# Optimization experiments

Measured on AMD Instinct MI355X. Metric: run time of the kernel, lower is better.

Reference implementation:

```python
import jax, jax.numpy as jnp
import numpy as np

V, D, H, L, E, DH, K, PMAX = 50257, 128, 4, 4, 8, 512, 2, 256
B, T = 8, 256


def setup_inputs() -> dict:
    key = jax.random.key(0)
    ks = jax.random.split(key, 10)
    s = 0.02
    def n(k, shape):
        return jax.random.normal(k, shape, jnp.float32) * s
    return dict(
        idx=jax.random.randint(ks[0], (B, T), 0, V),
        tok_emb=n(ks[1], (V, D)),
        pos_emb=n(ks[2], (PMAX, D)),
        ln1_g=jnp.ones((L, D), jnp.float32), ln1_b=jnp.zeros((L, D), jnp.float32),
        in_w=n(ks[3], (L, 3 * D, D)), in_b=jnp.zeros((L, 3 * D), jnp.float32),
        out_w=n(ks[4], (L, D, D)), out_b=jnp.zeros((L, D), jnp.float32),
        ln2_g=jnp.ones((L, D), jnp.float32), ln2_b=jnp.zeros((L, D), jnp.float32),
        gate_w=n(ks[5], (L, E, D)),
        w1=n(ks[6], (L, E, DH, D)),
        w2=n(ks[7], (L, E, D, DH)),
        lnf_g=jnp.ones((D,), jnp.float32), lnf_b=jnp.zeros((D,), jnp.float32),
        lm_w=n(ks[8], (V, D)),
    )


def _ln(x, g, b):
    mu = x.mean(-1, keepdims=True)
    var = jnp.var(x, -1, keepdims=True)
    return (x - mu) / jnp.sqrt(var + 1e-5) * g + b


def _moe(x, gw, w1, w2):
    # x: [N, D]; top-2 sparse MoE, computed densely per expert then combined.
    logits = x @ gw.T                              # [N, E]
    probs = jax.nn.softmax(logits, -1)
    topw, topi = jax.lax.top_k(probs, K)           # [N, K]
    topw = topw / topw.sum(-1, keepdims=True)
    we = (topw[..., None] * jax.nn.one_hot(topi, E, dtype=x.dtype)).sum(1)  # [N, E]
    h = jax.nn.silu(jnp.einsum('nd,ehd->neh', x, w1))   # [N, E, DH]
    y = jnp.einsum('neh,edh->ned', h, w2)               # [N, E, D]
    return jnp.einsum('ned,ne->nd', y, we)


def reference(idx, tok_emb, pos_emb, ln1_g, ln1_b, in_w, in_b, out_w, out_b,
              ln2_g, ln2_b, gate_w, w1, w2, lnf_g, lnf_b, lm_w):
    b, t = idx.shape
    x = tok_emb[idx] + pos_emb[:t]                 # [B, T, D]
    dh = D // H
    scale = 1.0 / np.sqrt(dh)
    for l in range(L):
        xl = _ln(x, ln1_g[l], ln1_b[l])
        qkv = xl @ in_w[l].T + in_b[l]
        q, k, v = jnp.split(qkv, 3, -1)
        q = q.reshape(b, t, H, dh)
        k = k.reshape(b, t, H, dh)
        v = v.reshape(b, t, H, dh)
        att = jax.nn.softmax(jnp.einsum('bqhd,bkhd->bhqk', q, k) * scale, -1)
        o = jnp.einsum('bhqk,bkhd->bqhd', att, v).reshape(b, t, D)
        x = x + o @ out_w[l].T + out_b[l]
        x2 = _ln(x, ln2_g[l], ln2_b[l]).reshape(b * t, D)
        x = x + _moe(x2, gate_w[l], w1[l], w2[l]).reshape(b, t, D)
    return _ln(x, lnf_g, lnf_b) @ lm_w.T           # [B, T, V]
```

## Files before the change

### kernel.cpp

```cpp
#include <hip/hip_runtime.h>
#include <math.h>

#define NTOK 2048
#define DD   128
#define NHEAD 4
#define DHEAD 32
#define NLAYER 4
#define NEXP 8
#define DHID 512
#define NVOCAB 50257
#define VPAD  50304
#define SEQ   256
#define NBATCH 8

typedef __attribute__((ext_vector_type(8))) short short8v;
typedef __attribute__((ext_vector_type(4))) float f32x4;

__device__ __forceinline__ unsigned short nm_bf16r(float f) {
  unsigned u = __float_as_uint(f);
  u += 0x7fffu + ((u >> 16) & 1u);
  return (unsigned short)(u >> 16);
}

__device__ __forceinline__ float nm_silu(float a) {
  return a / (1.f + __expf(-a));
}

template<int N4>
__device__ __forceinline__ float nm_dotv(const float* __restrict__ a,
                                         const float* __restrict__ w) {
  const float4* a4 = (const float4*)a;
  const float4* w4 = (const float4*)w;
  float sx = 0.f, sy = 0.f, sz = 0.f, sw = 0.f;
#pragma unroll 16
  for (int k = 0; k < N4; ++k) {
    float4 av = a4[k], wv = w4[k];
    sx = fmaf(av.x, wv.x, sx);
    sy = fmaf(av.y, wv.y, sy);
    sz = fmaf(av.z, wv.z, sz);
    sw = fmaf(av.w, wv.w, sw);
  }
  return (sx + sy) + (sz + sw);
}

#define C3_LMW 6438912ull
#define C3_W1  6963200ull
#define C3_ALL 7487488ull
#define CVTB   7312
__global__ __launch_bounds__(256) void nm_init(
    const int* __restrict__ idx, const float* __restrict__ tok,
    const float* __restrict__ pos, const float* __restrict__ g,
    const float* __restrict__ b, const float* __restrict__ lmw,
    const float* __restrict__ w1l3, const float* __restrict__ w2l3,
    float* __restrict__ x, float* __restrict__ xl,
    unsigned short* __restrict__ lmwb, unsigned short* __restrict__ w1b3,
    unsigned short* __restrict__ w2b3, int* __restrict__ zp) {
  int bid = blockIdx.x, tid = threadIdx.x;
  if (bid < CVTB) {
    size_t base = ((size_t)bid * 256 + tid) * 4;
    if (base < (size_t)NVOCAB * DD) {
      float4 v = *(const float4*)(lmw + base);
      ushort4 us = {nm_bf16r(v.x), nm_bf16r(v.y), nm_bf16r(v.z), nm_bf16r(v.w)};
      *(ushort4*)(lmwb + base) = us;
    } else if (base < C3_LMW) {
      ushort4 us = {0, 0, 0, 0};
      *(ushort4*)(lmwb + base) = us;
    } else if (base < C3_W1) {
      size_t j = base - C3_LMW;
      float4 v = *(const float4*)(w1l3 + j);
      ushort4 us = {nm_bf16r(v.x), nm_bf16r(v.y), nm_bf16r(v.z), nm_bf16r(v.w)};
      *(ushort4*)(w1b3 + j) = us;
    } else {
      size_t j = base - C3_W1;
      float4 v = *(const float4*)(w2l3 + j);
      ushort4 us = {nm_bf16r(v.x), nm_bf16r(v.y), nm_bf16r(v.z), nm_bf16r(v.w)};
      *(ushort4*)(w2b3 + j) = us;
    }
  } else if (bid < CVTB + NTOK / 4) {
    int n = (bid - CVTB) * 4 + (tid >> 6);
    int lane = tid & 63;
    int t = idx[n];
    float v0 = tok[(size_t)t * DD + lane]      + pos[(n % SEQ) * DD + lane];
    float v1 = tok[(size_t)t * DD + lane + 64] + pos[(n % SEQ) * DD + lane + 64];
    x[n * DD + lane]      = v0;
    x[n * DD + lane + 64] = v1;
    float s = v0 + v1;
#pragma unroll
    for (int o = 32; o > 0; o >>= 1) s += __shfl_xor(s, o, 64);
    float mu = s * (1.f / 128.f);
    float d0 = v0 - mu, d1 = v1 - mu;
    float q = d0 * d0 + d1 * d1;
#pragma unroll
    for (int o = 32; o > 0; o >>= 1) q += __shfl_xor(q, o, 64);
    float rstd = rsqrtf(q * (1.f / 128.f) + 1e-5f);
    xl[n * DD + lane]      = d0 * rstd * g[lane]      + b[lane];
    xl[n * DD + lane + 64] = d1 * rstd * g[lane + 64] + b[lane + 64];
  } else {
    if (tid < 68) zp[tid] = 0;
  }
}

__global__ void nm_embed_ln(const int* __restrict__ idx, const float* __restrict__ tok,
                            const float* __restrict__ pos, const float* __restrict__ g,
                            const float* __restrict__ b, float* __restrict__ x,
                            float* __restrict__ xlf) {
  int n = blockIdx.x, lane = threadIdx.x;
  int t = idx[n];
  float v0 = tok[(size_t)t * DD + lane]      + pos[(n % SEQ) * DD + lane];
  float v1 = tok[(size_t)t * DD + lane + 64] + pos[(n % SEQ) * DD + lane + 64];
  x[n * DD + lane]      = v0;
  x[n * DD + lane + 64] = v1;
  float s = v0 + v1;
#pragma unroll
  for (int o = 32; o > 0; o >>= 1) s += __shfl_xor(s, o, 64);
  float mu = s * (1.f / 128.f);
  float d0 = v0 - mu, d1 = v1 - mu;
  float q = d0 * d0 + d1 * d1;
#pragma unroll
  for (int o = 32; o > 0; o >>= 1) q += __shfl_xor(q, o, 64);
  float rstd = rsqrtf(q * (1.f / 128.f) + 1e-5f);
  xlf[n * DD + lane]      = d0 * rstd * g[lane]      + b[lane];
  xlf[n * DD + lane + 64] = d1 * rstd * g[lane + 64] + b[lane + 64];
}

__global__ void nm_ln(const float* __restrict__ in, const float* __restrict__ g,
                      const float* __restrict__ b, float* __restrict__ out) {
  int n = blockIdx.x, lane = threadIdx.x;
  float v0 = in[n * DD + lane], v1 = in[n * DD + lane + 64];
  float s = v0 + v1;
#pragma unroll
  for (int o = 32; o > 0; o >>= 1) s += __shfl_xor(s, o, 64);
  float mu = s * (1.f / 128.f);
  float d0 = v0 - mu, d1 = v1 - mu;
  float q = d0 * d0 + d1 * d1;
#pragma unroll
  for (int o = 32; o > 0; o >>= 1) q += __shfl_xor(q, o, 64);
  float rstd = rsqrtf(q * (1.f / 128.f) + 1e-5f);
  out[n * DD + lane]      = d0 * rstd * g[lane]      + b[lane];
  out[n * DD + lane + 64] = d1 * rstd * g[lane + 64] + b[lane + 64];
}

__global__ void nm_combine_ln(const float* __restrict__ yb, const int* __restrict__ posm,
                              const float* __restrict__ topw, float* __restrict__ x,
                              const float* __restrict__ g, const float* __restrict__ b,
                              float* __restrict__ xl, unsigned short* __restrict__ xb) {
  int n = blockIdx.x, lane = threadIdx.x;
  float w0 = topw[2 * n], w1 = topw[2 * n + 1];
  int p0 = posm[2 * n], p1 = posm[2 * n + 1];
  float v0 = x[n * DD + lane]      + w0 * yb[(size_t)p0 * DD + lane]
                                   + w1 * yb[(size_t)p1 * DD + lane];
  float v1 = x[n * DD + lane + 64] + w0 * yb[(size_t)p0 * DD + lane + 64]
                                   + w1 * yb[(size_t)p1 * DD + lane + 64];
  x[n * DD + lane]      = v0;
  x[n * DD + lane + 64] = v1;
  float s = v0 + v1;
#pragma unroll
  for (int o = 32; o > 0; o >>= 1) s += __shfl_xor(s, o, 64);
  float mu = s * (1.f / 128.f);
  float d0 = v0 - mu, d1 = v1 - mu;
  float q = d0 * d0 + d1 * d1;
#pragma unroll
  for (int o = 32; o > 0; o >>= 1) q += __shfl_xor(q, o, 64);
  float rstd = rsqrtf(q * (1.f / 128.f) + 1e-5f);
  float o0 = d0 * rstd * g[lane]      + b[lane];
  float o1 = d1 * rstd * g[lane + 64] + b[lane + 64];
  xl[n * DD + lane]      = o0;
  xl[n * DD + lane + 64] = o1;
  if (xb) {
    xb[n * DD + lane]      = nm_bf16r(o0);
    xb[n * DD + lane + 64] = nm_bf16r(o1);
  }
}

template<int F, int MT>
__global__ __launch_bounds__(256) void nm_gemm2(
    const float* __restrict__ A, const float* __restrict__ B,
    float* __restrict__ C, const float* __restrict__ bias,
    int M, int N, int K,
    const int* __restrict__ list, const int* __restrict__ cnt,
    const int* __restrict__ off) {
  constexpr bool GA = F & 1, SI = F & 2, BI = F & 4, GR = F & 16;
  constexpr int RG = MT / 64;
  __shared__ __align__(16) float As[64][MT + 4];
  __shared__ __align__(16) float Bs[64][68];
  int tid = threadIdx.x;
  int n0 = blockIdx.x * 64, m0 = blockIdx.y * MT;
  int Mloc = M, o = 0;
  const float* Bb = B;
  if constexpr (GR) {
    int e = blockIdx.z;
    Mloc = cnt[e];
    if (m0 >= Mloc) return;
    o = off[e];
    Bb = B + (size_t)e * (size_t)N * K;
  }
  int tm = tid & 15, tn = tid >> 4;
  float acc[RG * 4][4] = {};
  for (int kc = 0; kc < K; kc += 64) {
#pragma unroll
    for (int i = 0; i < RG * 4; ++i) {
      int f = tid + 256 * i;
      int r = f >> 4, c4 = f & 15;
      int mi = m0 + r;
      if (mi >= Mloc) mi = m0;
      const float* ar;
      if constexpr (GA) ar = A + (size_t)(list[o + mi] >> 1) * K;
      else              ar = A + (size_t)(o + mi) * K;
      float4 v = *(const float4*)(ar + kc + c4 * 4);
      int k = c4 * 4;
      As[k][r] = v.x; As[k + 1][r] = v.y; As[k + 2][r] = v.z; As[k + 3][r] = v.w;
    }
#pragma unroll
    for (int i = 0; i < 4; ++i) {
      int f = tid + 256 * i;
      int r = f >> 4, c4 = f & 15;
      const float* br = Bb + (size_t)(n0 + r) * K + kc + c4 * 4;
      float4 v = *(const float4*)br;
      int k = c4 * 4;
      Bs[k][r] = v.x; Bs[k + 1][r] = v.y; Bs[k + 2][r] = v.z; Bs[k + 3][r] = v.w;
    }
    __syncthreads();
#pragma unroll 16
    for (int k = 0; k < 64; ++k) {
      float4 b = *(const float4*)&Bs[k][tn * 4];
#pragma unroll
      for (int g2 = 0; g2 < RG; ++g2) {
        float4 a = *(const float4*)&As[k][g2 * 64 + tm * 4];
        acc[g2*4+0][0] = fmaf(a.x, b.x, acc[g2*4+0][0]);
        acc[g2*4+0][1] = fmaf(a.x, b.y, acc[g2*4+0][1]);
        acc[g2*4+0][2] = fmaf(a.x, b.z, acc[g2*4+0][2]);
        acc[g2*4+0][3] = fmaf(a.x, b.w, acc[g2*4+0][3]);
        acc[g2*4+1][0] = fmaf(a.y, b.x, acc[g2*4+1][0]);
        acc[g2*4+1][1] = fmaf(a.y, b.y, acc[g2*4+1][1]);
        acc[g2*4+1][2] = fmaf(a.y, b.z, acc[g2*4+1][2]);
        acc[g2*4+1][3] = fmaf(a.y, b.w, acc[g2*4+1][3]);
        acc[g2*4+2][0] = fmaf(a.z, b.x, acc[g2*4+2][0]);
        acc[g2*4+2][1] = fmaf(a.z, b.y, acc[g2*4+2][1]);
        acc[g2*4+2][2] = fmaf(a.z, b.z, acc[g2*4+2][2]);
        acc[g2*4+2][3] = fmaf(a.z, b.w, acc[g2*4+2][3]);
        acc[g2*4+3][0] = fmaf(a.w, b.x, acc[g2*4+3][0]);
        acc[g2*4+3][1] = fmaf(a.w, b.y, acc[g2*4+3][1]);
        acc[g2*4+3][2] = fmaf(a.w, b.z, acc[g2*4+3][2]);
        acc[g2*4+3][3] = fmaf(a.w, b.w, acc[g2*4+3][3]);
      }
    }
    __syncthreads();
  }
  float4 bv = {0.f, 0.f, 0.f, 0.f};
  if constexpr (BI) bv = *(const float4*)(bias + n0 + tn * 4);
#pragma unroll
  for (int g2 = 0; g2 < RG; ++g2) {
#pragma unroll
    for (int i = 0; i < 4; ++i) {
      int row = m0 + g2 * 64 + tm * 4 + i;
      if (GR && row >= Mloc) continue;
      float* cr = C + (size_t)(o + row) * N + n0 + tn * 4;
      float r0 = acc[g2 * 4 + i][0], r1 = acc[g2 * 4 + i][1];
      float r2 = acc[g2 * 4 + i][2], r3 = acc[g2 * 4 + i][3];
      if constexpr (BI) { r0 += bv.x; r1 += bv.y; r2 += bv.z; r3 += bv.w; }
      if constexpr (SI) { r0 = nm_silu(r0); r1 = nm_silu(r1); r2 = nm_silu(r2); r3 = nm_silu(r3); }
      float4 st = {r0, r1, r2, r3};
      *(float4*)cr = st;
    }
  }
}

template<int F, int KK>
__global__ __launch_bounds__(256) void nm_bgemm(
    const unsigned short* __restrict__ A, const unsigned short* __restrict__ B,
    float* __restrict__ Cf, unsigned short* __restrict__ Cb,
    const float* __restrict__ bias, int M, int N,
    const int* __restrict__ list, const int* __restrict__ cnt,
    const int* __restrict__ off) {
  constexpr bool GA = F & 1, SI = F & 2, BI = F & 4, SB = F & 8, GR = F & 16;
  int wave = threadIdx.x >> 6, lane = threadIdx.x & 63;
  int n0 = blockIdx.x * 32;
  int m0 = blockIdx.y * 128 + wave * 32;
  int Mloc = M, o = 0;
  const unsigned short* Bb = B;
  if constexpr (GR) {
    int e = blockIdx.z;
    Mloc = cnt[e];
    o = off[e];
    Bb = B + (size_t)e * (size_t)N * KK;
  }
  if (m0 >= Mloc) return;
  int lr = lane & 15, lk = (lane >> 4) * 8;
  const unsigned short* arow[2];
#pragma unroll
  for (int i = 0; i < 2; ++i) {
    int mi = m0 + i * 16 + lr;
    if (mi >= Mloc) mi = Mloc - 1;
    int r = GA ? (list[o + mi] >> 1) : (o + mi);
    arow[i] = A + (size_t)r * KK;
  }
  const unsigned short* brow[2] = { Bb + (size_t)(n0 + lr) * KK,
                                    Bb + (size_t)(n0 + 16 + lr) * KK };
  f32x4 acc[2][2] = {};
#pragma unroll
  for (int ks = 0; ks < KK / 32; ++ks) {
    int kb = ks * 32 + lk;
    short8v a0 = *(const short8v*)(arow[0] + kb);
    short8v a1 = *(const short8v*)(arow[1] + kb);
    short8v b0 = *(const short8v*)(brow[0] + kb);
    short8v b1 = *(const short8v*)(brow[1] + kb);
    acc[0][0] = __builtin_amdgcn_mfma_f32_16x16x32_bf16(a0, b0, acc[0][0], 0, 0, 0);
    acc[0][1] = __builtin_amdgcn_mfma_f32_16x16x32_bf16(a0, b1, acc[0][1], 0, 0, 0);
    acc[1][0] = __builtin_amdgcn_mfma_f32_16x16x32_bf16(a1, b0, acc[1][0], 0, 0, 0);
    acc[1][1] = __builtin_amdgcn_mfma_f32_16x16x32_bf16(a1, b1, acc[1][1], 0, 0, 0);
  }
  float bc[2] = {0.f, 0.f};
  if constexpr (BI) {
    bc[0] = bias[n0 + (lane & 15)];
    bc[1] = bias[n0 + 16 + (lane & 15)];
  }
#pragma unroll
  for (int i = 0; i < 2; ++i) {
    int rbase = m0 + i * 16 + (lane >> 4) * 4;
#pragma unroll
    for (int r = 0; r < 4; ++r) {
      int row = rbase + r;
      if (GR && row >= Mloc) continue;
#pragma unroll
      for (int j = 0; j < 2; ++j) {
        float v = acc[i][j][r];
        if constexpr (BI) v += bc[j];
        if constexpr (SI) v = nm_silu(v);
        int col = n0 + j * 16 + (lane & 15);
        if constexpr (SB) Cb[(size_t)(o + row) * N + col] = nm_bf16r(v);
        else              Cf[(size_t)(o + row) * N + col] = v;
      }
    }
  }
}

__global__ __launch_bounds__(256) void nm_oplng(
    const float* __restrict__ ao, const float* __restrict__ w,
    const float* __restrict__ bias, float* __restrict__ x,
    const float* __restrict__ g, const float* __restrict__ b,
    float* __restrict__ xlf, unsigned short* __restrict__ xlb,
    const float* __restrict__ gw,
    int* __restrict__ topi, float* __restrict__ topw, int* __restrict__ cnt,
    int* __restrict__ ticket, int* __restrict__ off, int* __restrict__ list,
    int* __restrict__ posm) {
  __shared__ __align__(16) float As[64][36];
  __shared__ __align__(16) float Bs[64][132];
  __shared__ float Ls[32][9];
  __shared__ int doR;
  __shared__ int cv[NEXP], lcur[NEXP];
  int tid = threadIdx.x;
  int m0 = blockIdx.x * 32;
  int tm = tid >> 5, tn = tid & 31;
  float acc[4][4] = {};
  for (int kc = 0; kc < DD; kc += 64) {
#pragma unroll
    for (int i = 0; i < 2; ++i) {
      int ch = tid + 256 * i, r = ch >> 4, c4 = ch & 15;
      float4 v = *(const float4*)(ao + (size_t)(m0 + r) * DD + kc + c4 * 4);
      int k = c4 * 4;
      As[k][r] = v.x; As[k + 1][r] = v.y; As[k + 2][r] = v.z; As[k + 3][r] = v.w;
    }
#pragma unroll
    for (int i = 0; i < 8; ++i) {
      int ch = tid + 256 * i, r = ch >> 4, c4 = ch & 15;
      float4 v = *(const float4*)(w + (size_t)r * DD + kc + c4 * 4);
      int k = c4 * 4;
      Bs[k][r] = v.x; Bs[k + 1][r] = v.y; Bs[k + 2][r] = v.z; Bs[k + 3][r] = v.w;
    }
    __syncthreads();
#pragma unroll 8
    for (int k = 0; k < 64; ++k) {
      float4 a = *(const float4*)&As[k][tm * 4];
      float4 bb = *(const float4*)&Bs[k][tn * 4];
      acc[0][0] = fmaf(a.x, bb.x, acc[0][0]); acc[0][1] = fmaf(a.x, bb.y, acc[0][1]);
      acc[0][2] = fmaf(a.x, bb.z, acc[0][2]); acc[0][3] = fmaf(a.x, bb.w, acc[0][3]);
      acc[1][0] = fmaf(a.y, bb.x, acc[1][0]); acc[1][1] = fmaf(a.y, bb.y, acc[1][1]);
      acc[1][2] = fmaf(a.y, bb.z, acc[1][2]); acc[1][3] = fmaf(a.y, bb.w, acc[1][3]);
      acc[2][0] = fmaf(a.z, bb.x, acc[2][0]); acc[2][1] = fmaf(a.z, bb.y, acc[2][1]);
      acc[2][2] = fmaf(a.z, bb.z, acc[2][2]); acc[2][3] = fmaf(a.z, bb.w, acc[2][3]);
      acc[3][0] = fmaf(a.w, bb.x, acc[3][0]); acc[3][1] = fmaf(a.w, bb.y, acc[3][1]);
      acc[3][2] = fmaf(a.w, bb.z, acc[3][2]); acc[3][3] = fmaf(a.w, bb.w, acc[3][3]);
    }
    __syncthreads();
  }
  float4 bv = *(const float4*)(bias + tn * 4);
  float rr[4][4], s1[4], s2[4];
#pragma unroll
  for (int i = 0; i < 4; ++i) {
    int rw = m0 + tm * 4 + i;
    float4 xv = *(const float4*)(x + (size_t)rw * DD + tn * 4);
    float r0 = acc[i][0] + bv.x + xv.x;
    float r1 = acc[i][1] + bv.y + xv.y;
    float r2 = acc[i][2] + bv.z + xv.z;
    float r3 = acc[i][3] + bv.w + xv.w;
    rr[i][0] = r0; rr[i][1] = r1; rr[i][2] = r2; rr[i][3] = r3;
    float4 st = {r0, r1, r2, r3};
    *(float4*)(x + (size_t)rw * DD + tn * 4) = st;
    s1[i] = r0 + r1 + r2 + r3;
    s2[i] = r0 * r0 + r1 * r1 + r2 * r2 + r3 * r3;
  }
#pragma unroll
  for (int o = 16; o >= 1; o >>= 1) {
#pragma unroll
    for (int i = 0; i < 4; ++i) {
      s1[i] += __shfl_xor(s1[i], o, 64);
      s2[i] += __shfl_xor(s2[i], o, 64);
    }
  }
  float4 gv  = *(const float4*)(g + tn * 4);
  float4 bbv = *(const float4*)(b + tn * 4);
#pragma unroll
  for (int i = 0; i < 4; ++i) {
    int rw = m0 + tm * 4 + i;
    float mu = s1[i] * (1.f / 128.f);
    float var = s2[i] * (1.f / 128.f) - mu * mu;
    float rstd = rsqrtf(var + 1e-5f);
    float y0 = (rr[i][0] - mu) * rstd * gv.x + bbv.x;
    float y1 = (rr[i][1] - mu) * rstd * gv.y + bbv.y;
    float y2 = (rr[i][2] - mu) * rstd * gv.z + bbv.z;
    float y3 = (rr[i][3] - mu) * rstd * gv.w + bbv.w;
    float4 yv = {y0, y1, y2, y3};
    if (xlf) *(float4*)(xlf + (size_t)rw * DD + tn * 4) = yv;
    if (xlb) {
      ushort4 us = {nm_bf16r(y0), nm_bf16r(y1), nm_bf16r(y2), nm_bf16r(y3)};
      *(ushort4*)(xlb + (size_t)rw * DD + tn * 4) = us;
    }
    *(float4*)&Bs[tm * 4 + i][tn * 4] = yv;
  }
  __syncthreads();
  int grow = tid >> 3, ge = tid & 7;
  const float4* xr = (const float4*)&Bs[grow][0];
  const float4* wr = (const float4*)(gw + (size_t)ge * DD);
  float sx = 0.f, sy = 0.f, sz = 0.f, sw = 0.f;
#pragma unroll
  for (int k2 = 0; k2 < 32; ++k2) {
    float4 a = xr[k2], w4 = wr[k2];
    sx = fmaf(a.x, w4.x, sx); sy = fmaf(a.y, w4.y, sy);
    sz = fmaf(a.z, w4.z, sz); sw = fmaf(a.w, w4.w, sw);
  }
  Ls[grow][ge] = (sx + sy) + (sz + sw);
  __syncthreads();
  if (ge == 0) {
    float gl[NEXP];
#pragma unroll
    for (int e = 0; e < NEXP; ++e) gl[e] = Ls[grow][e];
    int i0 = 0;
#pragma unroll
    for (int e = 1; e < NEXP; ++e) if (gl[e] > gl[i0]) i0 = e;
    int i1 = (i0 == 0) ? 1 : 0;
#pragma unroll
    for (int e = 0; e < NEXP; ++e) { if (e != i0 && gl[e] > gl[i1]) i1 = e; }
    float p1 = __expf(gl[i1] - gl[i0]);
    float inv = 1.f / (1.f + p1);
    int n = m0 + grow;
    topi[2 * n] = i0; topi[2 * n + 1] = i1;
    topw[2 * n] = inv; topw[2 * n + 1] = p1 * inv;
    atomicAdd(cnt + i0, 1);
    atomicAdd(cnt + i1, 1);
  }
  __syncthreads();
  if (tid == 0) {
    __threadfence();
    doR = (atomicAdd(ticket, 1) == 63);
    if (doR) __threadfence();
  }
  __syncthreads();
  if (doR) {
    if (tid < NEXP) cv[tid] = atomicAdd(cnt + tid, 0);
    __syncthreads();
    if (tid < NEXP) {
      int o2 = 0;
      for (int e = 0; e < tid; ++e) o2 += cv[e];
      lcur[tid] = o2;
      off[tid] = o2;
    }
    __syncthreads();
    for (int t = tid; t < 2 * NTOK; t += 256) {
      int e = topi[t];
      int p = atomicAdd(&lcur[e], 1);
// ... 42 lines not shown
    float sc = 0.f;
#pragma unroll
    for (int k = 0; k < 8; ++k) {
      float4 v = kr[k];
      sc += qv[4*k]*v.x + qv[4*k+1]*v.y + qv[4*k+2]*v.z + qv[4*k+3]*v.w;
    }
    sc *= scale;
    float mn = fmaxf(m, sc);
    float f = __expf(m - mn), p = __expf(sc - mn);
    s = s * f + p;
    const float4* vr = (const float4*)Vs[j];
#pragma unroll
    for (int k = 0; k < 8; ++k) {
      float4 v = vr[k];
      acc[4*k]   = acc[4*k]  * f + p * v.x;
      acc[4*k+1] = acc[4*k+1]* f + p * v.y;
      acc[4*k+2] = acc[4*k+2]* f + p * v.z;
      acc[4*k+3] = acc[4*k+3]* f + p * v.w;
    }
    m = mn;
  }
  mbuf[q][slot] = m;
  sbuf[q][slot] = s;
  __syncthreads();
  float M = mbuf[q][0];
#pragma unroll
  for (int t = 1; t < 8; ++t) M = fmaxf(M, mbuf[q][t]);
  float S = 0.f;
#pragma unroll
  for (int t = 0; t < 8; ++t) S += sbuf[q][t] * __expf(mbuf[q][t] - M);
  float w = __expf(m - M);
#pragma unroll
  for (int d = 0; d < DHEAD; ++d) acc[d] *= w;
#pragma unroll
  for (int p = 0; p < 8; ++p) {
    if (slot == p) {
      if (p == 0) {
#pragma unroll
        for (int d = 0; d < DHEAD; ++d) accbuf[q][d] = acc[d];
      } else {
#pragma unroll
        for (int d = 0; d < DHEAD; ++d) accbuf[q][d] += acc[d];
      }
    }
    __syncthreads();
  }
  if (slot == 0) sbuf[q][8] = 1.f / S;
  __syncthreads();
  int q2 = tid >> 3, c4 = tid & 7;
  float inv = sbuf[q2][8];
  float4 v = *(const float4*)&accbuf[q2][c4 * 4];
  v.x *= inv; v.y *= inv; v.z *= inv; v.w *= inv;
  *(float4*)(o + (size_t)(b * SEQ + qt * 32 + q2) * DD + h * DHEAD + c4 * 4) = v;
}

__global__ void nm_qkv(const float* __restrict__ xl, const float* __restrict__ w,
                       const float* __restrict__ bias, float* __restrict__ qkv) {
  __shared__ __align__(16) float xs[DD];
  int n = blockIdx.x, tid = threadIdx.x;
  xs[tid] = xl[n * DD + tid];
  __syncthreads();
#pragma unroll
  for (int jj = 0; jj < 3; ++jj) {
    int j = tid + jj * 128;
    qkv[(size_t)n * 384 + j] = nm_dotv<32>(xs, w + (size_t)j * DD) + bias[j];
  }
}

__global__ void nm_outproj(const float* __restrict__ ao, const float* __restrict__ w,
                           const float* __restrict__ bias, float* __restrict__ x) {
  __shared__ __align__(16) float os[DD];
  int n = blockIdx.x, tid = threadIdx.x;
  os[tid] = ao[n * DD + tid];
  __syncthreads();
  x[n * DD + tid] += nm_dotv<32>(os, w + (size_t)tid * DD) + bias[tid];
}

__global__ void nm_moe(const float* __restrict__ x2, const float* __restrict__ gw,
                       const float* __restrict__ w1, const float* __restrict__ w2,
                       float* __restrict__ x) {
  __shared__ __align__(16) float xs[DD];
  __shared__ __align__(16) float hs[DHID];
  __shared__ float gl[NEXP];
  __shared__ int   ei[2];
  __shared__ float ew[2];
  int n = blockIdx.x, tid = threadIdx.x;
  if (tid < DD) xs[tid] = x2[n * DD + tid];
  __syncthreads();
  if (tid < NEXP) gl[tid] = nm_dotv<32>(xs, gw + (size_t)tid * DD);
  __syncthreads();
  if (tid == 0) {
    int i0 = 0;
#pragma unroll
    for (int e = 1; e < NEXP; ++e) if (gl[e] > gl[i0]) i0 = e;
    int i1 = (i0 == 0) ? 1 : 0;
    for (int e = 0; e < NEXP; ++e) { if (e == i0) continue; if (gl[e] > gl[i1]) i1 = e; }
    float p1 = __expf(gl[i1] - gl[i0]);
    float inv = 1.f / (1.f + p1);
    ei[0] = i0; ei[1] = i1; ew[0] = inv; ew[1] = p1 * inv;
  }
  __syncthreads();
  float yacc = 0.f;
  for (int t2 = 0; t2 < 2; ++t2) {
    int e = ei[t2];
    float wt = ew[t2];
    const float* w1e = w1 + (size_t)e * DHID * DD;
// ... 114 lines not shown
#pragma unroll
  for (int j = 0; j < 4; ++j)
#pragma unroll
    for (int i = 0; i < 4; ++i)
#pragma unroll
      for (int r = 0; r < 4; ++r)
        Cs[(wr * 64 + i * 16 + hi4 + r) * 132 + wc * 64 + j * 16 + lr] = acc[i][j][r];
  __syncthreads();
  bool full = (col0 + 128 <= NVOCAB);
#pragma unroll 4
  for (int rr = 0; rr < 32; ++rr) {
    int row = wave * 32 + rr;
    float v0 = Cs[row * 132 + lane];
    float v1 = Cs[row * 132 + 64 + lane];
    size_t base = (size_t)(row0 + row) * NVOCAB + col0;
    if (full) {
      out[base + lane] = v0;
      out[base + 64 + lane] = v1;
    } else {
      if (col0 + lane < NVOCAB)      out[base + lane] = v0;
      if (col0 + 64 + lane < NVOCAB) out[base + 64 + lane] = v1;
    }
  }
}

extern "C" void kernel_launch(void* const* d_in, const int* in_sizes, int n_in,
                              void* d_out, int out_size, void* d_ws, size_t ws_size,
                              hipStream_t stream) {
  const int*   idx   = (const int*)  d_in[0];
  const float* tok   = (const float*)d_in[1];
  const float* pos   = (const float*)d_in[2];
  const float* ln1g  = (const float*)d_in[3];
  const float* ln1b  = (const float*)d_in[4];
  const float* inw   = (const float*)d_in[5];
  const float* inb   = (const float*)d_in[6];
  const float* outw  = (const float*)d_in[7];
  const float* outb  = (const float*)d_in[8];
  const float* ln2g  = (const float*)d_in[9];
  const float* ln2b  = (const float*)d_in[10];
  const float* gatew = (const float*)d_in[11];
  const float* w1    = (const float*)d_in[12];
  const float* w2    = (const float*)d_in[13];
  const float* lnfg  = (const float*)d_in[14];
  const float* lnfb  = (const float*)d_in[15];
  const float* lmw   = (const float*)d_in[16];
  float* out = (float*)d_out;

  float* ws   = (float*)d_ws;
  float* x    = ws;
  float* xl   = x    + NTOK * DD;
  float* qkv  = xl   + NTOK * DD;
  float* ao   = qkv  + NTOK * 384;
  float* topw = ao   + NTOK * DD;
  float* H    = topw + 2 * NTOK;
  float* yb   = H    + 2 * NTOK * DHID;
  int*   topi = (int*)(yb + 2 * NTOK * DD);
  int*   list = topi + 2 * NTOK;
  int*   posm = list + 2 * NTOK;
  int*   cnt  = posm + 2 * NTOK;
  int*   offs = cnt  + NLAYER * NEXP;
  int*   tick = offs + NLAYER * NEXP;
  unsigned short* xlb  = (unsigned short*)(tick + 8);
  unsigned short* Hb   = xlb + NTOK * DD;
  unsigned short* xfb  = Hb  + 2 * NTOK * DHID;
  unsigned short* w1b3 = xfb + NTOK * DD;
  unsigned short* w2b3 = w1b3 + NEXP * DHID * DD;
  unsigned short* lmwb = w2b3 + NEXP * DD * DHID;
  const size_t need = (size_t)((char*)(lmwb + (size_t)VPAD * DD) - (char*)d_ws);
  const bool pre = (ws_size >= need);

  const float* w1l3 = w1 + (size_t)3 * NEXP * DHID * DD;
  const float* w2l3 = w2 + (size_t)3 * NEXP * DD * DHID;

  if (pre) {
    nm_init<<<CVTB + NTOK / 4 + 1, 256, 0, stream>>>(
        idx, tok, pos, ln1g, ln1b, lmw, w1l3, w2l3, x, xl, lmwb, w1b3, w2b3, cnt);
    for (int l = 0; l < NLAYER; ++l) {
      nm_gemm2<4, 128><<<dim3(384 / 64, NTOK / 128), 256, 0, stream>>>(
          xl, inw + (size_t)l * 384 * DD, qkv, inb + (size_t)l * 384,
          NTOK, 384, DD, nullptr, nullptr, nullptr);
      nm_attn2<<<dim3(NBATCH * NHEAD, SEQ / 32), 256, 0, stream>>>(qkv, ao);
      nm_oplng<<<NTOK / 32, 256, 0, stream>>>(
          ao, outw + (size_t)l * DD * DD, outb + (size_t)l * DD, x,
          ln2g + l * DD, ln2b + l * DD, xl, (l == 3) ? xlb : (unsigned short*)nullptr,
          gatew + (size_t)l * NEXP * DD, topi, topw, cnt + l * NEXP,
          tick + l, offs + l * NEXP, list, posm);
      int* cnt_l = cnt + l * NEXP;
      int* off_l = offs + l * NEXP;
      if (l < 3) {
        const float* w1l = w1 + (size_t)l * NEXP * DHID * DD;
        const float* w2l = w2 + (size_t)l * NEXP * DD * DHID;
        nm_gemm2<19, 128><<<dim3(DHID / 64, 2 * NTOK / 128, NEXP), 256, 0, stream>>>(
            xl, w1l, H, nullptr, 0, DHID, DD, list, cnt_l, off_l);
        nm_gemm2<16, 64><<<dim3(DD / 64, 2 * NTOK / 64, NEXP), 256, 0, stream>>>(
            H, w2l, yb, nullptr, 0, DD, DHID, nullptr, cnt_l, off_l);
      } else {
        nm_bgemm<27, 128><<<dim3(DHID / 32, 32, NEXP), 256, 0, stream>>>(
            xlb, w1b3, nullptr, Hb, nullptr, 0, DHID, list, cnt_l, off_l);
        nm_bgemm<16, 512><<<dim3(DD / 32, 32, NEXP), 256, 0, stream>>>(
            Hb, w2b3, yb, nullptr, nullptr, 0, DD, nullptr, cnt_l, off_l);
      }
      const float* gN = (l < NLAYER - 1) ? ln1g + (l + 1) * DD : lnfg;
      const float* bN = (l < NLAYER - 1) ? ln1b + (l + 1) * DD : lnfb;
      nm_combine_ln<<<NTOK, 64, 0, stream>>>(
          yb, posm, topw, x, gN, bN, xl,
          (l == NLAYER - 1) ? xfb : (unsigned short*)nullptr);
    }
    nm_lmhead2<<<dim3(VPAD / 128, NTOK / 128), 256, 0, stream>>>(xfb, lmwb, out);
  } else {
    nm_embed_ln<<<NTOK, 64, 0, stream>>>(idx, tok, pos, ln1g, ln1b, x, xl);
    for (int l = 0; l < NLAYER; ++l) {
      nm_qkv<<<NTOK, 128, 0, stream>>>(xl, inw + (size_t)l * 384 * DD,
                                       inb + (size_t)l * 384, qkv);
      nm_attn2<<<dim3(NBATCH * NHEAD, SEQ / 32), 256, 0, stream>>>(qkv, ao);
      nm_outproj<<<NTOK, 128, 0, stream>>>(ao, outw + (size_t)l * DD * DD,
                                           outb + (size_t)l * DD, x);
      nm_ln<<<NTOK, 64, 0, stream>>>(x, ln2g + l * DD, ln2b + l * DD, xl);
      nm_moe<<<NTOK, 256, 0, stream>>>(xl, gatew + (size_t)l * NEXP * DD,
                                       w1 + (size_t)l * NEXP * DHID * DD,
                                       w2 + (size_t)l * NEXP * DD * DHID, x);
      const float* gN = (l < NLAYER - 1) ? ln1g + (l + 1) * DD : lnfg;
      const float* bN = (l < NLAYER - 1) ? ln1b + (l + 1) * DD : lnfb;
      nm_ln<<<NTOK, 64, 0, stream>>>(x, gN, bN, xl);
    }
    nm_lmhead_f32<<<dim3(VPAD / 128, NTOK / 128), 256, 0, stream>>>(xl, lmw, out);
  }
}
```

Before: 828.4 us.

## Fuse combine+LN with QKV projection and expert FFN into single MoE kernel

```diff
diff --git a/kernel.cpp b/kernel.cpp
--- a/kernel.cpp
+++ b/kernel.cpp
@@ -43,18 +43,14 @@
   return (sx + sy) + (sz + sw);
 }
 
-#define C3_LMW 6438912ull
-#define C3_W1  6963200ull
-#define C3_ALL 7487488ull
-#define CVTB   7312
+#define CVT_N 6438912ull
+#define CVTB  6288
 __global__ __launch_bounds__(256) void nm_init(
     const int* __restrict__ idx, const float* __restrict__ tok,
     const float* __restrict__ pos, const float* __restrict__ g,
     const float* __restrict__ b, const float* __restrict__ lmw,
-    const float* __restrict__ w1l3, const float* __restrict__ w2l3,
     float* __restrict__ x, float* __restrict__ xl,
-    unsigned short* __restrict__ lmwb, unsigned short* __restrict__ w1b3,
-    unsigned short* __restrict__ w2b3, int* __restrict__ zp) {
+    unsigned short* __restrict__ lmwb, int* __restrict__ zp) {
   int bid = blockIdx.x, tid = threadIdx.x;
   if (bid < CVTB) {
     size_t base = ((size_t)bid * 256 + tid) * 4;
@@ -62,19 +58,9 @@
       float4 v = *(const float4*)(lmw + base);
       ushort4 us = {nm_bf16r(v.x), nm_bf16r(v.y), nm_bf16r(v.z), nm_bf16r(v.w)};
       *(ushort4*)(lmwb + base) = us;
-    } else if (base < C3_LMW) {
+    } else {
       ushort4 us = {0, 0, 0, 0};
       *(ushort4*)(lmwb + base) = us;
-    } else if (base < C3_W1) {
-      size_t j = base - C3_LMW;
-      float4 v = *(const float4*)(w1l3 + j);
-      ushort4 us = {nm_bf16r(v.x), nm_bf16r(v.y), nm_bf16r(v.z), nm_bf16r(v.w)};
-      *(ushort4*)(w1b3 + j) = us;
-    } else {
-      size_t j = base - C3_W1;
-      float4 v = *(const float4*)(w2l3 + j);
-      ushort4 us = {nm_bf16r(v.x), nm_bf16r(v.y), nm_bf16r(v.z), nm_bf16r(v.w)};
-      *(ushort4*)(w2b3 + j) = us;
     }
   } else if (bid < CVTB + NTOK / 4) {
     int n = (bid - CVTB) * 4 + (tid >> 6);
@@ -96,241 +82,147 @@
     xl[n * DD + lane]      = d0 * rstd * g[lane]      + b[lane];
     xl[n * DD + lane + 64] = d1 * rstd * g[lane + 64] + b[lane + 64];
   } else {
-    if (tid < 68) zp[tid] = 0;
-  }
-}
-
-__global__ void nm_embed_ln(const int* __restrict__ idx, const float* __restrict__ tok,
-                            const float* __restrict__ pos, const float* __restrict__ g,
-                            const float* __restrict__ b, float* __restrict__ x,
-                            float* __restrict__ xlf) {
-  int n = blockIdx.x, lane = threadIdx.x;
-  int t = idx[n];
-  float v0 = tok[(size_t)t * DD + lane]      + pos[(n % SEQ) * DD + lane];
-  float v1 = tok[(size_t)t * DD + lane + 64] + pos[(n % SEQ) * DD + lane + 64];
-  x[n * DD + lane]      = v0;
-  x[n * DD + lane + 64] = v1;
-  float s = v0 + v1;
-#pragma unroll
-  for (int o = 32; o > 0; o >>= 1) s += __shfl_xor(s, o, 64);
-  float mu = s * (1.f / 128.f);
-  float d0 = v0 - mu, d1 = v1 - mu;
-  float q = d0 * d0 + d1 * d1;
-#pragma unroll
-  for (int o = 32; o > 0; o >>= 1) q += __shfl_xor(q, o, 64);
-  float rstd = rsqrtf(q * (1.f / 128.f) + 1e-5f);
-  xlf[n * DD + lane]      = d0 * rstd * g[lane]      + b[lane];
-  xlf[n * DD + lane + 64] = d1 * rstd * g[lane + 64] + b[lane + 64];
-}
-
-__global__ void nm_ln(const float* __restrict__ in, const float* __restrict__ g,
-                      const float* __restrict__ b, float* __restrict__ out) {
-  int n = blockIdx.x, lane = threadIdx.x;
-  float v0 = in[n * DD + lane], v1 = in[n * DD + lane + 64];
-  float s = v0 + v1;
-#pragma unroll
-  for (int o = 32; o > 0; o >>= 1) s += __shfl_xor(s, o, 64);
-  float mu = s * (1.f / 128.f);
-  float d0 = v0 - mu, d1 = v1 - mu;
-  float q = d0 * d0 + d1 * d1;
-#pragma unroll
-  for (int o = 32; o > 0; o >>= 1) q += __shfl_xor(q, o, 64);
-  float rstd = rsqrtf(q * (1.f / 128.f) + 1e-5f);
-  out[n * DD + lane]      = d0 * rstd * g[lane]      + b[lane];
-  out[n * DD + lane + 64] = d1 * rstd * g[lane + 64] + b[lane + 64];
-}
-
-__global__ void nm_combine_ln(const float* __restrict__ yb, const int* __restrict__ posm,
-                              const float* __restrict__ topw, float* __restrict__ x,
-                              const float* __restrict__ g, const float* __restrict__ b,
-                              float* __restrict__ xl, unsigned short* __restrict__ xb) {
-  int n = blockIdx.x, lane = threadIdx.x;
-  float w0 = topw[2 * n], w1 = topw[2 * n + 1];
-  int p0 = posm[2 * n], p1 = posm[2 * n + 1];
-  float v0 = x[n * DD + lane]      + w0 * yb[(size_t)p0 * DD + lane]
-                                   + w1 * yb[(size_t)p1 * DD + lane];
-  float v1 = x[n * DD + lane + 64] + w0 * yb[(size_t)p0 * DD + lane + 64]
-                                   + w1 * yb[(size_t)p1 * DD + lane + 64];
-  x[n * DD + lane]      = v0;
-  x[n * DD + lane + 64] = v1;
-  float s = v0 + v1;
-#pragma unroll
-  for (int o = 32; o > 0; o >>= 1) s += __shfl_xor(s, o, 64);
-  float mu = s * (1.f / 128.f);
-  float d0 = v0 - mu, d1 = v1 - mu;
-  float q = d0 * d0 + d1 * d1;
-#pragma unroll
-  for (int o = 32; o > 0; o >>= 1) q += __shfl_xor(q, o, 64);
-  float rstd = rsqrtf(q * (1.f / 128.f) + 1e-5f);
-  float o0 = d0 * rstd * g[lane]      + b[lane];
-  float o1 = d1 * rstd * g[lane + 64] + b[lane + 64];
-  xl[n * DD + lane]      = o0;
-  xl[n * DD + lane + 64] = o1;
-  if (xb) {
-    xb[n * DD + lane]      = nm_bf16r(o0);
-    xb[n * DD + lane + 64] = nm_bf16r(o1);
-  }
-}
-
-template<int F, int MT>
-__global__ __launch_bounds__(256) void nm_gemm2(
-    const float* __restrict__ A, const float* __restrict__ B,
-    float* __restrict__ C, const float* __restrict__ bias,
-    int M, int N, int K,
-    const int* __restrict__ list, const int* __restrict__ cnt,
-    const int* __restrict__ off) {
-  constexpr bool GA = F & 1, SI = F & 2, BI = F & 4, GR = F & 16;
-  constexpr int RG = MT / 64;
-  __shared__ __align__(16) float As[64][MT + 4];
-  __shared__ __align__(16) float Bs[64][68];
+    if (tid < 72) zp[tid] = 0;
+  }
+}
+
+template<int MODE>
+__global__ __launch_bounds__(256) void nm_cqkv(
+    const float* __restrict__ yb, const int* __restrict__ posm,
+    const float* __restrict__ topw, float* __restrict__ x,
+    const float* __restrict__ xlin, const float* __restrict__ g,
+    const float* __restrict__ b, unsigned short* __restrict__ xfb,
+    const float* __restrict__ w, const float* __restrict__ bias,
+    float* __restrict__ qkv) {
+  __shared__ __align__(16) float xs[32][132];
+  __shared__ __align__(16) float qs[(MODE < 2) ? 32 * 388 : 4];
   int tid = threadIdx.x;
-  int n0 = blockIdx.x * 64, m0 = blockIdx.y * MT;
-  int Mloc = M, o = 0;
-  const float* Bb = B;
-  if constexpr (GR) {
-    int e = blockIdx.z;
-    Mloc = cnt[e];
-    if (m0 >= Mloc) return;
-    o = off[e];
-    Bb = B + (size_t)e * (size_t)N * K;
-  }
-  int tm = tid & 15, tn = tid >> 4;
-  float acc[RG * 4][4] = {};
-  for (int kc = 0; kc < K; kc += 64) {
-#pragma unroll
-    for (int i = 0; i < RG * 4; ++i) {
-      int f = tid + 256 * i;
-      int r = f >> 4, c4 = f & 15;
-      int mi = m0 + r;
-      if (mi >= Mloc) mi = m0;
-      const float* ar;
-      if constexpr (GA) ar = A + (size_t)(list[o + mi] >> 1) * K;
-      else              ar = A + (size_t)(o + mi) * K;
-      float4 v = *(const float4*)(ar + kc + c4 * 4);
-      int k = c4 * 4;
-      As[k][r] = v.x; As[k + 1][r] = v.y; As[k + 2][r] = v.z; As[k + 3][r] = v.w;
-    }
+  int n0 = blockIdx.x * 32;
+  int r = tid >> 3, p = tid & 7;
+  int n = n0 + r;
+  float4 a0, a1, a2, a3;
+  if constexpr (MODE == 0) {
+    const float* xr = xlin + (size_t)n * DD + p * 16;
+    a0 = *(const float4*)(xr + 0);  a1 = *(const float4*)(xr + 4);
+    a2 = *(const float4*)(xr + 8);  a3 = *(const float4*)(xr + 12);
 #pragma unroll
     for (int i = 0; i < 4; ++i) {
-      int f = tid + 256 * i;
-      int r = f >> 4, c4 = f & 15;
-      const float* br = Bb + (size_t)(n0 + r) * K + kc + c4 * 4;
-      float4 v = *(const float4*)br;
-      int k = c4 * 4;
-      Bs[k][r] = v.x; Bs[k + 1][r] = v.y; Bs[k + 2][r] = v.z; Bs[k + 3][r] = v.w;
-    }
-    __syncthreads();
-#pragma unroll 16
-    for (int k = 0; k < 64; ++k) {
-      float4 b = *(const float4*)&Bs[k][tn * 4];
-#pragma unroll
-      for (int g2 = 0; g2 < RG; ++g2) {
-        float4 a = *(const float4*)&As[k][g2 * 64 + tm * 4];
-        acc[g2*4+0][0] = fmaf(a.x, b.x, acc[g2*4+0][0]);
-        acc[g2*4+0][1] = fmaf(a.x, b.y, acc[g2*4+0][1]);
-        acc[g2*4+0][2] = fmaf(a.x, b.z, acc[g2*4+0][2]);
-        acc[g2*4+0][3] = fmaf(a.x, b.w, acc[g2*4+0][3]);
-        acc[g2*4+1][0] = fmaf(a.y, b.x, acc[g2*4+1][0]);
-        acc[g2*4+1][1] = fmaf(a.y, b.y, acc[g2*4+1][1]);
-        acc[g2*4+1][2] = fmaf(a.y, b.z, acc[g2*4+1][2]);
-        acc[g2*4+1][3] = fmaf(a.y, b.w, acc[g2*4+1][3]);
-        acc[g2*4+2][0] = fmaf(a.z, b.x, acc[g2*4+2][0]);
-        acc[g2*4+2][1] = fmaf(a.z, b.y, acc[g2*4+2][1]);
-        acc[g2*4+2][2] = fmaf(a.z, b.z, acc[g2*4+2][2]);
-        acc[g2*4+2][3] = fmaf(a.z, b.w, acc[g2*4+2][3]);
-        acc[g2*4+3][0] = fmaf(a.w, b.x, acc[g2*4+3][0]);
-        acc[g2*4+3][1] = fmaf(a.w, b.y, acc[g2*4+3][1]);
-        acc[g2*4+3][2] = fmaf(a.w, b.z, acc[g2*4+3][2]);
-        acc[g2*4+3][3] = fmaf(a.w, b.w, acc[g2*4+3][3]);
+      ((float4*)&xs[r][p * 16])[i] = (i == 0) ? a0 : (i == 1) ? a1 : (i == 2) ? a2 : a3;
+    }
+  } else {
+    float* xr = x + (size_t)n * DD + p * 16;
+    a0 = *(const float4*)(xr + 0);  a1 = *(const float4*)(xr + 4);
+    a2 = *(const float4*)(xr + 8);  a3 = *(const float4*)(xr + 12);
+    float w0 = topw[2 * n], w1 = topw[2 * n + 1];
+    int p0 = posm[2 * n], p1 = posm[2 * n + 1];
+    const float* y0 = yb + (size_t)p0 * DD + p * 16;
+    const float* y1 = yb + (size_t)p1 * DD + p * 16;
+#pragma unroll
+    for (int i = 0; i < 4; ++i) {
+      float4 u0 = ((const float4*)y0)[i];
+      float4 u1 = ((const float4*)y1)[i];
+      float4* ai = (i == 0) ? &a0 : (i == 1) ? &a1 : (i == 2) ? &a2 : &a3;
+      ai->x += w0 * u0.x + w1 * u1.x;
+      ai->y += w0 * u0.y + w1 * u1.y;
+      ai->z += w0 * u0.z + w1 * u1.z;
+      ai->w += w0 * u0.w + w1 * u1.w;
+    }
+    if constexpr (MODE == 1) {
+      ((float4*)xr)[0] = a0; ((float4*)xr)[1] = a1;
+      ((float4*)xr)[2] = a2; ((float4*)xr)[3] = a3;
+    }
+    float s1 = (a0.x + a0.y + a0.z + a0.w) + (a1.x + a1.y + a1.z + a1.w)
+             + (a2.x + a2.y + a2.z + a2.w) + (a3.x + a3.y + a3.z + a3.w);
+    float s2 = a0.x*a0.x + a0.y*a0.y + a0.z*a0.z + a0.w*a0.w
+             + a1.x*a1.x + a1.y*a1.y + a1.z*a1.z + a1.w*a1.w
+             + a2.x*a2.x + a2.y*a2.y + a2.z*a2.z + a2.w*a2.w
+             + a3.x*a3.x + a3.y*a3.y + a3.z*a3.z + a3.w*a3.w;
+#pragma unroll
+    for (int o = 4; o >= 1; o >>= 1) {
+      s1 += __shfl_xor(s1, o, 8);
+      s2 += __shfl_xor(s2, o, 8);
+    }
+    float mu = s1 * (1.f / 128.f);
+    float var = s2 * (1.f / 128.f) - mu * mu;
+    float rstd = rsqrtf(var + 1e-5f);
+    const float4* gp = (const float4*)(g + p * 16);
+    const float4* bp = (const float4*)(b + p * 16);
+#pragma unroll
+    for (int i = 0; i < 4; ++i) {
+      float4 gv = gp[i], bv = bp[i];
+      float4* ai = (i == 0) ? &a0 : (i == 1) ? &a1 : (i == 2) ? &a2 : &a3;
+      float4 yv = {(ai->x - mu) * rstd * gv.x + bv.x,
+                   (ai->y - mu) * rstd * gv.y + bv.y,
+                   (ai->z - mu) * rstd * gv.z + bv.z,
+                   (ai->w - mu) * rstd * gv.w + bv.w};
+      if constexpr (MODE == 2) {
+        ushort4 us = {nm_bf16r(yv.x), nm_bf16r(yv.y), nm_bf16r(yv.z), nm_bf16r(yv.w)};
+        *(ushort4*)(xfb + (size_t)n * DD + p * 16 + i * 4) = us;
+      } else {
+        ((float4*)&xs[r][p * 16])[i] = yv;
       }
     }
-    __syncthreads();
-  }
-  float4 bv = {0.f, 0.f, 0.f, 0.f};
-  if constexpr (BI) bv = *(const float4*)(bias + n0 + tn * 4);
-#pragma unroll
-  for (int g2 = 0; g2 < RG; ++g2) {
-#pragma unroll
-    for (int i = 0; i < 4; ++i) {
-      int row = m0 + g2 * 64 + tm * 4 + i;
-      if (GR && row >= Mloc) continue;
-      float* cr = C + (size_t)(o + row) * N + n0 + tn * 4;
-      float r0 = acc[g2 * 4 + i][0], r1 = acc[g2 * 4 + i][1];
-      float r2 = acc[g2 * 4 + i][2], r3 = acc[g2 * 4 + i][3];
-      if constexpr (BI) { r0 += bv.x; r1 += bv.y; r2 += bv.z; r3 += bv.w; }
-      if constexpr (SI) { r0 = nm_silu(r0); r1 = nm_silu(r1); r2 = nm_silu(r2); r3 = nm_silu(r3); }
-      float4 st = {r0, r1, r2, r3};
-      *(float4*)cr = st;
-    }
-  }
-}
-
-template<int F, int KK>
-__global__ __launch_bounds__(256) void nm_bgemm(
-    const unsigned short* __restrict__ A, const unsigned short* __restrict__ B,
-    float* __restrict__ Cf, unsigned short* __restrict__ Cb,
-    const float* __restrict__ bias, int M, int N,
-    const int* __restrict__ list, const int* __restrict__ cnt,
-    const int* __restrict__ off) {
-  constexpr bool GA = F & 1, SI = F & 2, BI = F & 4, SB = F & 8, GR = F & 16;
-  int wave = threadIdx.x >> 6, lane = threadIdx.x & 63;
-  int n0 = blockIdx.x * 32;
-  int m0 = blockIdx.y * 128 + wave * 32;
-  int Mloc = M, o = 0;
-  const unsigned short* Bb = B;
-  if constexpr (GR) {
-    int e = blockIdx.z;
-    Mloc = cnt[e];
-    o = off[e];
-    Bb = B + (size_t)e * (size_t)N * KK;
-  }
-  if (m0 >= Mloc) return;
-  int lr = lane & 15, lk = (lane >> 4) * 8;
-  const unsigned short* arow[2];
+  }
+  if constexpr (MODE == 2) return;
+  __syncthreads();
+  float* qsf = (float*)qs;
+#pragma unroll 8
+  for (int i = 0; i < 48; ++i) {
+    int pp = i * 256 + tid;
+    int col = pp >> 5, tk = pp & 31;
+    float v = nm_dotv<32>(&xs[tk][0], w + (size_t)col * DD) + bias[col];
+    qsf[tk * 388 + col] = v;
+  }
+  __syncthreads();
+#pragma unroll
+  for (int i = 0; i < 12; ++i) {
+    int e4 = i * 256 + tid;
+    int tk = e4 / 96, c4 = e4 % 96;
+    float4 v = *(const float4*)&qsf[tk * 388 + c4 * 4];
+    *(float4*)(qkv + (size_t)(n0 + tk) * 384 + c4 * 4) = v;
+  }
+}
+
+__global__ __launch_bounds__(256) void nm_moe_f(
+    const float* __restrict__ xl, const float* __restrict__ w1,
+    const float* __restrict__ w2, const int* __restrict__ list,
+    const int* __restrict__ cnt, const int* __restrict__ off,
+    float* __restrict__ yb) {
+  __shared__ __align__(16) float xs[16][132];
+  __shared__ __align__(16) float Hs[16][516];
+  int e = blockIdx.y;
+  int c = cnt[e];
+  int m0 = blockIdx.x * 16;
+  if (m0 >= c) return;
+  int o = off[e];
+  const float* w1e = w1 + (size_t)e * DHID * DD;
+  const float* w2e = w2 + (size_t)e * DD * DHID;
+  int tid = threadIdx.x;
 #pragma unroll
   for (int i = 0; i < 2; ++i) {
-    int mi = m0 + i * 16 + lr;
-    if (mi >= Mloc) mi = Mloc - 1;
-    int r = GA ? (list[o + mi] >> 1) : (o + mi);
-    arow[i] = A + (size_t)r * KK;
-  }
-  const unsigned short* brow[2] = { Bb + (size_t)(n0 + lr) * KK,
-                                    Bb + (size_t)(n0 + 16 + lr) * KK };
-  f32x4 acc[2][2] = {};
-#pragma unroll
-  for (int ks = 0; ks < KK / 32; ++ks) {
-    int kb = ks * 32 + lk;
-    short8v a0 = *(const short8v*)(arow[0] + kb);
-    short8v a1 = *(const short8v*)(arow[1] + kb);
-    short8v b0 = *(const short8v*)(brow[0] + kb);
-    short8v b1 = *(const short8v*)(brow[1] + kb);
-    acc[0][0] = __builtin_amdgcn_mfma_f32_16x16x32_bf16(a0, b0, acc[0][0], 0, 0, 0);
-    acc[0][1] = __builtin_amdgcn_mfma_f32_16x16x32_bf16(a0, b1, acc[0][1], 0, 0, 0);
-    acc[1][0] = __builtin_amdgcn_mfma_f32_16x16x32_bf16(a1, b0, acc[1][0], 0, 0, 0);
-    acc[1][1] = __builtin_amdgcn_mfma_f32_16x16x32_bf16(a1, b1, acc[1][1], 0, 0, 0);
-  }
-  float bc[2] = {0.f, 0.f};
-  if constexpr (BI) {
-    bc[0] = bias[n0 + (lane & 15)];
-    bc[1] = bias[n0 + 16 + (lane & 15)];
-  }
-#pragma unroll
-  for (int i = 0; i < 2; ++i) {
-    int rbase = m0 + i * 16 + (lane >> 4) * 4;
-#pragma unroll
-    for (int r = 0; r < 4; ++r) {
-      int row = rbase + r;
-      if (GR && row >= Mloc) continue;
-#pragma unroll
-      for (int j = 0; j < 2; ++j) {
-        float v = acc[i][j][r];
-        if constexpr (BI) v += bc[j];
-        if constexpr (SI) v = nm_silu(v);
-        int col = n0 + j * 16 + (lane & 15);
-        if constexpr (SB) Cb[(size_t)(o + row) * N + col] = nm_bf16r(v);
-        else              Cf[(size_t)(o + row) * N + col] = v;
-      }
-    }
+    int f = tid + 256 * i;
+    int row = f >> 5, c4 = f & 31;
+    int mi = m0 + row;
+    if (mi >= c) mi = m0;
+    int tk = list[o + mi] >> 1;
+    *(float4*)&xs[row][c4 * 4] = *(const float4*)(xl + (size_t)tk * DD + c4 * 4);
+  }
+  __syncthreads();
+  int r = tid >> 4, cg = tid & 15;
+#pragma unroll 4
+  for (int jj = 0; jj < 32; ++jj) {
+    int j = jj * 16 + cg;
+    float a = nm_dotv<32>(&xs[r][0], w1e + (size_t)j * DD);
+    Hs[r][j] = nm_silu(a);
+  }
+  __syncthreads();
+  int row = m0 + r;
+  bool ok = (row < c);
+#pragma unroll
+  for (int cc = 0; cc < 8; ++cc) {
+    int col = cc * 16 + cg;
+    float a = nm_dotv<128>(&Hs[r][0], w2e + (size_t)col * DHID);
+    if (ok) yb[(size_t)(o + row) * DD + col] = a;
   }
 }
 
@@ -338,8 +230,7 @@
     const float* __restrict__ ao, const float* __restrict__ w,
     const float* __restrict__ bias, float* __restrict__ x,
     const float* __restrict__ g, const float* __restrict__ b,
-    float* __restrict__ xlf, unsigned short* __restrict__ xlb,
-    const float* __restrict__ gw,
+    float* __restrict__ xl, const float* __restrict__ gw,
     int* __restrict__ topi, float* __restrict__ topw, int* __restrict__ cnt,
     int* __restrict__ ticket, int* __restrict__ off, int* __restrict__ list,
     int* __restrict__ posm) {
@@ -420,11 +311,7 @@
     float y2 = (rr[i][2] - mu) * rstd * gv.z + bbv.z;
     float y3 = (rr[i][3] - mu) * rstd * gv.w + bbv.w;
     float4 yv = {y0, y1, y2, y3};
-    if (xlf) *(float4*)(xlf + (size_t)rw * DD + tn * 4) = yv;
-    if (xlb) {
-      ushort4 us = {nm_bf16r(y0), nm_bf16r(y1), nm_bf16r(y2), nm_bf16r(y3)};
-      *(ushort4*)(xlb + (size_t)rw * DD + tn * 4) = us;
-    }
+    *(float4*)(xl + (size_t)rw * DD + tn * 4) = yv;
     *(float4*)&Bs[tm * 4 + i][tn * 4] = yv;
   }
   __syncthreads();
@@ -573,6 +460,46 @@
   float4 v = *(const float4*)&accbuf[q2][c4 * 4];
   v.x *= inv; v.y *= inv; v.z *= inv; v.w *= inv;
   *(float4*)(o + (size_t)(b * SEQ + qt * 32 + q2) * DD + h * DHEAD + c4 * 4) = v;
+}
+
+__global__ void nm_embed_ln(const int* __restrict__ idx, const float* __restrict__ tok,
+                            const float* __restrict__ pos, const float* __restrict__ g,
+                            const float* __restrict__ b, float* __restrict__ x,
+                            float* __restrict__ xlf) {
+  int n = blockIdx.x, lane = threadIdx.x;
+  int t = idx[n];
+  float v0 = tok[(size_t)t * DD + lane]      + pos[(n % SEQ) * DD + lane];
+  float v1 = tok[(size_t)t * DD + lane + 64] + pos[(n % SEQ) * DD + lane + 64];
+  x[n * DD + lane]      = v0;
+  x[n * DD + lane + 64] = v1;
+  float s = v0 + v1;
+#pragma unroll
+  for (int o = 32; o > 0; o >>= 1) s += __shfl_xor(s, o, 64);
+  float mu = s * (1.f / 128.f);
+  float d0 = v0 - mu, d1 = v1 - mu;
+  float q = d0 * d0 + d1 * d1;
+#pragma unroll
+  for (int o = 32; o > 0; o >>= 1) q += __shfl_xor(q, o, 64);
+  float rstd = rsqrtf(q * (1.f / 128.f) + 1e-5f);
+  xlf[n * DD + lane]      = d0 * rstd * g[lane]      + b[lane];
+  xlf[n * DD + lane + 64] = d1 * rstd * g[lane + 64] + b[lane + 64];
+}
+
+__global__ void nm_ln(const float* __restrict__ in, const float* __restrict__ g,
+                      const float* __restrict__ b, float* __restrict__ out) {
+  int n = blockIdx.x, lane = threadIdx.x;
+  float v0 = in[n * DD + lane], v1 = in[n * DD + lane + 64];
+  float s = v0 + v1;
+#pragma unroll
+  for (int o = 32; o > 0; o >>= 1) s += __shfl_xor(s, o, 64);
+  float mu = s * (1.f / 128.f);
+  float d0 = v0 - mu, d1 = v1 - mu;
+  float q = d0 * d0 + d1 * d1;
+#pragma unroll
+  for (int o = 32; o > 0; o >>= 1) q += __shfl_xor(q, o, 64);
+  float rstd = rsqrtf(q * (1.f / 128.f) + 1e-5f);
+  out[n * DD + lane]      = d0 * rstd * g[lane]      + b[lane];
+  out[n * DD + lane + 64] = d1 * rstd * g[lane + 64] + b[lane + 64];
 }
 
 __global__ void nm_qkv(const float* __restrict__ xl, const float* __restrict__ w,
@@ -793,59 +720,42 @@
   float* qkv  = xl   + NTOK * DD;
   float* ao   = qkv  + NTOK * 384;
   float* topw = ao   + NTOK * DD;
-  float* H    = topw + 2 * NTOK;
-  float* yb   = H    + 2 * NTOK * DHID;
+  float* yb   = topw + 2 * NTOK;
   int*   topi = (int*)(yb + 2 * NTOK * DD);
   int*   list = topi + 2 * NTOK;
   int*   posm = list + 2 * NTOK;
   int*   cnt  = posm + 2 * NTOK;
   int*   offs = cnt  + NLAYER * NEXP;
   int*   tick = offs + NLAYER * NEXP;
-  unsigned short* xlb  = (unsigned short*)(tick + 8);
-  unsigned short* Hb   = xlb + NTOK * DD;
-  unsigned short* xfb  = Hb  + 2 * NTOK * DHID;
-  unsigned short* w1b3 = xfb + NTOK * DD;
-  unsigned short* w2b3 = w1b3 + NEXP * DHID * DD;
-  unsigned short* lmwb = w2b3 + NEXP * DD * DHID;
+  unsigned short* xfb  = (unsigned short*)(tick + 8);
+  unsigned short* lmwb = xfb + NTOK * DD;
   const size_t need = (size_t)((char*)(lmwb + (size_t)VPAD * DD) - (char*)d_ws);
   const bool pre = (ws_size >= need);
 
-  const float* w1l3 = w1 + (size_t)3 * NEXP * DHID * DD;
-  const float* w2l3 = w2 + (size_t)3 * NEXP * DD * DHID;
-
   if (pre) {
     nm_init<<<CVTB + NTOK / 4 + 1, 256, 0, stream>>>(
-        idx, tok, pos, ln1g, ln1b, lmw, w1l3, w2l3, x, xl, lmwb, w1b3, w2b3, cnt);
+        idx, tok, pos, ln1g, ln1b, lmw, x, xl, lmwb, cnt);
+    nm_cqkv<0><<<NTOK / 32, 256, 0, stream>>>(
+        nullptr, nullptr, nullptr, x, xl, nullptr, nullptr, nullptr,
+        inw, inb, qkv);
     for (int l = 0; l < NLAYER; ++l) {
-      nm_gemm2<4, 128><<<dim3(384 / 64, NTOK / 128), 256, 0, stream>>>(
-          xl, inw + (size_t)l * 384 * DD, qkv, inb + (size_t)l * 384,
-          NTOK, 384, DD, nullptr, nullptr, nullptr);
       nm_attn2<<<dim3(NBATCH * NHEAD, SEQ / 32), 256, 0, stream>>>(qkv, ao);
       nm_oplng<<<NTOK / 32, 256, 0, stream>>>(
           ao, outw + (size_t)l * DD * DD, outb + (size_t)l * DD, x,
-          ln2g + l * DD, ln2b + l * DD, xl, (l == 3) ? xlb : (unsigned short*)nullptr,
-          gatew + (size_t)l * NEXP * DD, topi, topw, cnt + l * NEXP,
-          tick + l, offs + l * NEXP, list, posm);
-      int* cnt_l = cnt + l * NEXP;
-      int* off_l = offs + l * NEXP;
-      if (l < 3) {
-        const float* w1l = w1 + (size_t)l * NEXP * DHID * DD;
-        const float* w2l = w2 + (size_t)l * NEXP * DD * DHID;
-        nm_gemm2<19, 128><<<dim3(DHID / 64, 2 * NTOK / 128, NEXP), 256, 0, stream>>>(
-            xl, w1l, H, nullptr, 0, DHID, DD, list, cnt_l, off_l);
-        nm_gemm2<16, 64><<<dim3(DD / 64, 2 * NTOK / 64, NEXP), 256, 0, stream>>>(
-            H, w2l, yb, nullptr, 0, DD, DHID, nullptr, cnt_l, off_l);
+          ln2g + l * DD, ln2b + l * DD, xl, gatew + (size_t)l * NEXP * DD,
+          topi, topw, cnt + l * NEXP, tick + l, offs + l * NEXP, list, posm);
+      nm_moe_f<<<dim3(256, NEXP), 256, 0, stream>>>(
+          xl, w1 + (size_t)l * NEXP * DHID * DD, w2 + (size_t)l * NEXP * DD * DHID,
+          list, cnt + l * NEXP, offs + l * NEXP, yb);
+      if (l < NLAYER - 1) {
+        nm_cqkv<1><<<NTOK / 32, 256, 0, stream>>>(
+            yb, posm, topw, x, nullptr, ln1g + (l + 1) * DD, ln1b + (l + 1) * DD,
+            nullptr, inw + (size_t)(l + 1) * 384 * DD, inb + (size_t)(l + 1) * 384,
+            qkv);
       } else {
-        nm_bgemm<27, 128><<<dim3(DHID / 32, 32, NEXP), 256, 0, stream>>>(
-            xlb, w1b3, nullptr, Hb, nullptr, 0, DHID, list, cnt_l, off_l);
-        nm_bgemm<16, 512><<<dim3(DD / 32, 32, NEXP), 256, 0, stream>>>(
-            Hb, w2b3, yb, nullptr, nullptr, 0, DD, nullptr, cnt_l, off_l);
+        nm_cqkv<2><<<NTOK / 32, 256, 0, stream>>>(
+            yb, posm, topw, x, nullptr, lnfg, lnfb, xfb, nullptr, nullptr, nullptr);
       }
-      const float* gN = (l < NLAYER - 1) ? ln1g + (l + 1) * DD : lnfg;
-      const float* bN = (l < NLAYER - 1) ? ln1b + (l + 1) * DD : lnfb;
-      nm_combine_ln<<<NTOK, 64, 0, stream>>>(
-          yb, posm, topw, x, gN, bN, xl,
-          (l == NLAYER - 1) ? xfb : (unsigned short*)nullptr);
     }
     nm_lmhead2<<<dim3(VPAD / 128, NTOK / 128), 256, 0, stream>>>(xfb, lmwb, out);
   } else {
```

Result: slower. 3.312 ms (+299.8%).
